# Performance work log

Measured on AMD Instinct MI355X. Metric: run time of the kernel, lower is better.

The kernel has to match this reference:

```python
import jax, jax.numpy as jnp
import numpy as np

B, S, D_IN = 1, 2048, 2048
H, KV, HD = 32, 8, 64          # num_heads, num_kv_groups, head_dim
GS = H // KV                    # group_size
D_OUT = H * HD
EPS = 1e-6


def _rmsnorm(x, w):
    # RMSNormQwen over last dim (head_dim)
    var = jnp.mean(x * x, axis=-1, keepdims=True)
    return x * jax.lax.rsqrt(var + EPS) * w


def _rope(x, cos, sin):
    # rotate-half RoPE; x: [B, heads, S, HD], cos/sin: [S, HD]
    d = x.shape[-1]
    x1, x2 = x[..., : d // 2], x[..., d // 2 :]
    rot = jnp.concatenate([-x2, x1], axis=-1)
    return x * cos + rot * sin


def setup_inputs() -> dict:
    key = jax.random.key(0)
    ks = jax.random.split(key, 8)
    x = jax.random.normal(ks[0], (B, S, D_IN), dtype=jnp.float32)
    Wq = jax.random.normal(ks[1], (D_IN, D_OUT), dtype=jnp.float32) * 0.02
    Wk = jax.random.normal(ks[2], (D_IN, KV * HD), dtype=jnp.float32) * 0.02
    Wv = jax.random.normal(ks[3], (D_IN, KV * HD), dtype=jnp.float32) * 0.02
    Wo = jax.random.normal(ks[4], (D_OUT, D_IN), dtype=jnp.float32) * 0.02
    q_norm_w = jnp.ones((HD,), dtype=jnp.float32)
    k_norm_w = jnp.ones((HD,), dtype=jnp.float32)
    # causal mask: True where masked (j > i)
    mask = jnp.triu(jnp.ones((S, S), dtype=bool), k=1)
    # RoPE tables
    inv_freq = 1.0 / (10000.0 ** (np.arange(0, HD, 2, dtype=np.float32) / HD))
    ang = np.arange(S, dtype=np.float32)[:, None] * inv_freq[None, :]  # [S, HD/2]
    cos = jnp.asarray(np.concatenate([np.cos(ang), np.cos(ang)], axis=-1))
    sin = jnp.asarray(np.concatenate([np.sin(ang), np.sin(ang)], axis=-1))
    return {"x": x, "mask": mask, "cos": cos, "sin": sin,
            "Wq": Wq, "Wk": Wk, "Wv": Wv, "Wo": Wo,
            "q_norm_w": q_norm_w, "k_norm_w": k_norm_w}


def reference(x, mask, cos, sin, Wq, Wk, Wv, Wo, q_norm_w, k_norm_w):
    b, s, _ = x.shape
    q = (x @ Wq).reshape(b, s, H, HD).transpose(0, 2, 1, 3)   # [B,H,S,HD]
    k = (x @ Wk).reshape(b, s, KV, HD).transpose(0, 2, 1, 3)  # [B,KV,S,HD]
    v = (x @ Wv).reshape(b, s, KV, HD).transpose(0, 2, 1, 3)  # [B,KV,S,HD]
    q = _rmsnorm(q, q_norm_w)
    k = _rmsnorm(k, k_norm_w)
    q = _rope(q, cos, sin)
    k = _rope(k, cos, sin)
    # grouped-KV attention without materializing repeated K/V
    qg = q.reshape(b, KV, GS, s, HD)
    scores = jnp.einsum('bkgsd,bktd->bkgst', qg, k)           # [B,KV,GS,S,S]
    scores = jnp.where(mask, -jnp.inf, scores)
    weights = jax.nn.softmax(scores / (HD ** 0.5), axis=-1)
    ctx = jnp.einsum('bkgst,bktd->bkgsd', weights, v)         # [B,KV,GS,S,HD]
    ctx = ctx.reshape(b, H, s, HD).transpose(0, 2, 1, 3).reshape(b, s, D_OUT)
    return ctx @ Wo
```

## Files before the change

kernel.cpp:

```cpp
#include <hip/hip_runtime.h>
#include <hip/hip_bf16.h>
#include <math.h>

#define S_LEN 2048
#define DIN   2048
#define NH    32
#define NKV   8
#define HD    64
#define DOUT  2048
#define QKVN  3072
#define KOFF  2048
#define VOFF  2560

typedef __attribute__((ext_vector_type(8))) short short8v;
typedef __attribute__((ext_vector_type(8))) unsigned short ushort8v;
typedef __attribute__((ext_vector_type(4))) unsigned short ushort4v;
typedef __attribute__((ext_vector_type(4))) float float4v;
typedef __attribute__((ext_vector_type(16))) float float16v;

__device__ __forceinline__ float bf2f(unsigned short u) {
    union { float f; unsigned u; } c; c.u = ((unsigned)u) << 16; return c.f;
}
__device__ __forceinline__ unsigned short f2bf(float f) {
    union { float f; unsigned u; } c; c.f = f;
    unsigned r = c.u + 0x7fffu + ((c.u >> 16) & 1u);
    return (unsigned short)(r >> 16);
}
__device__ __forceinline__ unsigned short f2h(float f) {
    union { _Float16 h; unsigned short u; } c; c.h = (_Float16)f; return c.u;
}
__device__ __forceinline__ float h2f(unsigned short u) {
    union { _Float16 h; unsigned short u; } c; c.u = u; return (float)c.h;
}
__device__ __forceinline__ unsigned cvtpk(float lo, float hi) {
    unsigned r;
    asm("v_cvt_pk_bf16_f32 %0, %1, %2" : "=v"(r) : "v"(lo), "v"(hi));
    return r;
}
__device__ __forceinline__ float fexp2(float x) {
    float r;
    asm("v_exp_f32 %0, %1" : "=v"(r) : "v"(x));
    return r;
}

__global__ __launch_bounds__(256) void prep(const float* __restrict__ Wq,
                                            const float* __restrict__ Wk,
                                            const float* __restrict__ Wv,
                                            const float* __restrict__ Wo,
                                            const float* __restrict__ x,
                                            unsigned short* __restrict__ W1,
                                            unsigned short* __restrict__ WoT,
                                            unsigned short* __restrict__ XB) {
    __shared__ float t[32][33];
    const int a = blockIdx.x;
    const int tx = threadIdx.x & 31, ty = threadIdx.x >> 5;
    if (a < 6144) {
        const int n0 = (a % 96) * 32, k0 = (a / 96) * 32;
        const float* src; int nn0, Nsrc;
        if (n0 < KOFF)      { src = Wq; nn0 = n0;        Nsrc = DOUT; }
        else if (n0 < VOFF) { src = Wk; nn0 = n0 - KOFF; Nsrc = 512; }
        else                { src = Wv; nn0 = n0 - VOFF; Nsrc = 512; }
#pragma unroll
        for (int j = ty; j < 32; j += 8)
            t[j][tx] = src[(size_t)(k0 + j) * Nsrc + nn0 + tx];
        __syncthreads();
#pragma unroll
        for (int j = ty; j < 32; j += 8)
            W1[(size_t)(n0 + j) * DIN + k0 + tx] = f2bf(t[tx][j]);
    } else if (a < 10240) {
        const int b = a - 6144;
        const int n0 = (b % 64) * 32, k0 = (b / 64) * 32;
#pragma unroll
        for (int j = ty; j < 32; j += 8)
            t[j][tx] = Wo[(size_t)(k0 + j) * DIN + n0 + tx];
        __syncthreads();
#pragma unroll
        for (int j = ty; j < 32; j += 8)
            WoT[(size_t)(n0 + j) * DOUT + k0 + tx] = f2bf(t[tx][j]);
    } else {
        const int i = (a - 10240) * 1024 + threadIdx.x * 4;
        float4 v = *(const float4*)(x + i);
        XB[i + 0] = f2bf(v.x); XB[i + 1] = f2bf(v.y);
        XB[i + 2] = f2bf(v.z); XB[i + 3] = f2bf(v.w);
    }
}

template <int FUSE>
__global__ __launch_bounds__(256) void gemm64(const unsigned short* __restrict__ A,
                                              const unsigned short* __restrict__ Bt,
                                              void* __restrict__ Cv, int M, int N, int K,
                                              const float* __restrict__ qnw,
                                              const float* __restrict__ knw,
                                              const float* __restrict__ cosb,
                                              const float* __restrict__ sinb) {
    __shared__ __attribute__((aligned(16))) unsigned short As[2 * 128 * 64];
    __shared__ __attribute__((aligned(16))) unsigned short Bs[2 * 64 * 64];
    const int tid = threadIdx.x, lane = tid & 63, w = tid >> 6;
    const int bm = blockIdx.y * 128, bn = blockIdx.x * 64;
    const int wm = w * 32;

    float4v acc[2][4];
#pragma unroll
    for (int i = 0; i < 2; i++)
#pragma unroll
        for (int j = 0; j < 4; j++) acc[i][j] = (float4v){0.f, 0.f, 0.f, 0.f};

    const int srow = lane >> 3;
    const int schk = (lane & 7) ^ srow;
    const unsigned short* Ag[4];
    const unsigned short* Bg[2];
#pragma unroll
    for (int g = 0; g < 4; g++)
        Ag[g] = A + (size_t)(bm + w * 32 + g * 8 + srow) * K + schk * 8;
#pragma unroll
    for (int g = 0; g < 2; g++)
        Bg[g] = Bt + (size_t)(bn + w * 16 + g * 8 + srow) * K + schk * 8;

    auto STAGE = [&](int t, int b) {
        const size_t ko = (size_t)t * 64;
        unsigned short* Ad = As + b * (128 * 64) + (w * 32) * 64;
        unsigned short* Bd = Bs + b * (64 * 64) + (w * 16) * 64;
#pragma unroll
        for (int g = 0; g < 4; g++)
            __builtin_amdgcn_global_load_lds(
                (const __attribute__((address_space(1))) void*)(Ag[g] + ko),
                (__attribute__((address_space(3))) void*)(Ad + g * 8 * 64), 16, 0, 0);
#pragma unroll
        for (int g = 0; g < 2; g++)
            __builtin_amdgcn_global_load_lds(
                (const __attribute__((address_space(1))) void*)(Bg[g] + ko),
                (__attribute__((address_space(3))) void*)(Bd + g * 8 * 64), 16, 0, 0);
    };

    const int frow = lane & 15, quad = lane >> 4, sw = frow & 7;
    const int NT = K >> 6;

    STAGE(0, 0);

    for (int t = 0; t < NT; t++) {
        const int c = t & 1;
        if (t + 1 < NT) {
            STAGE(t + 1, c ^ 1);
            asm volatile("s_waitcnt vmcnt(6)" ::: "memory");
        } else {
            asm volatile("s_waitcnt vmcnt(0)" ::: "memory");
        }
        __builtin_amdgcn_s_barrier();
        __builtin_amdgcn_sched_barrier(0);

        const unsigned short* Ab = As + c * (128 * 64);
        const unsigned short* Bb = Bs + c * (64 * 64);
        short8v af[2][2], bf[4][2];
#pragma unroll
        for (int fm = 0; fm < 2; fm++)
#pragma unroll
            for (int ks = 0; ks < 2; ks++)
                af[fm][ks] = *(const short8v*)(Ab + (wm + fm * 16 + frow) * 64 +
                                               (((ks * 4 + quad) ^ sw) * 8));
#pragma unroll
        for (int fn = 0; fn < 4; fn++)
#pragma unroll
            for (int ks = 0; ks < 2; ks++)
                bf[fn][ks] = *(const short8v*)(Bb + (fn * 16 + frow) * 64 +
                                               (((ks * 4 + quad) ^ sw) * 8));
        __builtin_amdgcn_s_setprio(1);
#pragma unroll
        for (int ks = 0; ks < 2; ks++)
#pragma unroll
            for (int fm = 0; fm < 2; fm++)
#pragma unroll
                for (int fn = 0; fn < 4; fn++)
                    acc[fm][fn] = __builtin_amdgcn_mfma_f32_16x16x32_bf16(
                        af[fm][ks], bf[fn][ks], acc[fm][fn], 0, 0, 0);
        __builtin_amdgcn_s_setprio(0);

        if (t + 1 < NT) {
            asm volatile("s_waitcnt lgkmcnt(0)" ::: "memory");
            __builtin_amdgcn_sched_barrier(0);
            __builtin_amdgcn_s_barrier();
        }
    }

    const int quad4 = lane >> 4, col16 = lane & 15;
    if constexpr (FUSE == 1) {
        unsigned short* C = (unsigned short*)Cv;
        const int head = bn >> 6;
        if (head < 40) {
            const float* nw = (head < 32) ? qnw : knw;
            float wv[4];
#pragma unroll
            for (int fn = 0; fn < 4; fn++) wv[fn] = nw[fn * 16 + col16];
#pragma unroll
            for (int fm = 0; fm < 2; fm++)
#pragma unroll
                for (int r = 0; r < 4; r++) {
                    float x0 = acc[fm][0][r], x1 = acc[fm][1][r];
                    float x2 = acc[fm][2][r], x3 = acc[fm][3][r];
                    float ss = x0 * x0 + x1 * x1 + x2 * x2 + x3 * x3;
                    ss += __shfl_xor(ss, 1); ss += __shfl_xor(ss, 2);
                    ss += __shfl_xor(ss, 4); ss += __shfl_xor(ss, 8);
                    const float inv = rsqrtf(ss * (1.0f / 64.0f) + 1e-6f);
                    float xn[4] = {x0 * inv * wv[0], x1 * inv * wv[1],
                                   x2 * inv * wv[2], x3 * inv * wv[3]};
                    const int row = bm + wm + fm * 16 + quad4 * 4 + r;
                    const float* cr = cosb + (size_t)row * HD;
                    const float* sr = sinb + (size_t)row * HD;
#pragma unroll
                    for (int fn = 0; fn < 4; fn++) {
                        const float rot = (fn < 2) ? -xn[fn + 2] : xn[fn - 2];
                        const float res = xn[fn] * cr[fn * 16 + col16] +
                                          rot * sr[fn * 16 + col16];
                        C[(size_t)row * N + bn + fn * 16 + col16] = f2bf(res);
                    }
                }
        } else {
#pragma unroll
            for (int fm = 0; fm < 2; fm++)
#pragma unroll
                for (int fn = 0; fn < 4; fn++)
#pragma unroll
                    for (int r = 0; r < 4; r++)
                        C[(size_t)(bm + wm + fm * 16 + quad4 * 4 + r) * N +
                          bn + fn * 16 + col16] = f2bf(acc[fm][fn][r]);
        }
    } else {
        float* C = (float*)Cv;
#pragma unroll
        for (int fm = 0; fm < 2; fm++)
#pragma unroll
            for (int fn = 0; fn < 4; fn++)
#pragma unroll
                for (int r = 0; r < 4; r++)
                    C[(size_t)(bm + wm + fm * 16 + quad4 * 4 + r) * N +
                      bn + fn * 16 + col16] = acc[fm][fn][r];
    }
}

#define KSTR 88

__global__ __launch_bounds__(256, 3) void flash_part(const unsigned short* __restrict__ qb,
                                                     const unsigned short* __restrict__ kb,
                                                     const unsigned short* __restrict__ vb,
                                                     unsigned short* __restrict__ Op,
                                                     float* __restrict__ Lp) {
    __shared__ __attribute__((aligned(16))) unsigned short Ks[2][64 * KSTR];
    __shared__ __attribute__((aligned(16))) unsigned short Vt[2][64 * KSTR];

    const int tid = threadIdx.x, lane = tid & 63, w = tid >> 6;
    const int sl = lane & 31, hi = lane >> 5, hi8 = hi * 8;
    const int bid = blockIdx.x;
    const int g = bid & 7;
    const int p = (bid >> 3) & 31;
    const int c = bid >> 8;
    const int h = g * 4 + w;

    const int s0a = p * 32, s0b = (63 - p) * 32;
    const int nta = (s0a + 95) >> 6;
    const int W0 = c * 11;
    int nA = nta - W0;
    nA = nA < 0 ? 0 : (nA > 11 ? 11 : nA);
    const bool owesA = (c < 2);

    const float C1 = 0.18033688011112042f;
    const float C2 = 12.262908856239697f;

    unsigned short* OhA = Op + (size_t)c * 1024 * DOUT;
    float*          LhA = Lp + (size_t)c * 1024 * NH;
    unsigned short* OhB = Op + (size_t)(2 + c) * 1024 * DOUT;
    float*          LhB = Lp + (size_t)(2 + c) * 1024 * NH;

    int seg = owesA ? 0 : 1;
    int s0 = seg == 0 ? s0a : s0b;

    short8v qf[4];
#pragma unroll
    for (int ksq = 0; ksq < 4; ksq++)
        qf[ksq] = *(const short8v*)(qb + (size_t)(s0 + sl) * QKVN + h * HD +
                                    ksq * 16 + hi8);

    float16v O[2], Lacc;
#pragma unroll
    for (int df = 0; df < 2; df++)
#pragma unroll
        for (int r = 0; r < 16; r++) O[df][r] = 0.f;
#pragma unroll
    for (int r = 0; r < 16; r++) Lacc[r] = 0.f;

    short8v ones;
#pragma unroll
    for (int i = 0; i < 8; i++) ones[i] = (short)0x3F80;

    const int kkey = tid >> 2, kch = tid & 3;
    const unsigned short* kg = kb + (size_t)kkey * QKVN + g * HD + kch * 16;
    const int kp = tid & 31, vdbb = tid >> 5;
    const unsigned short* vg0 = vb + (size_t)(2 * kp) * QKVN + g * HD + vdbb * 8;
    const unsigned short* vg1 = vg0 + QKVN;

    auto epi = [&](int sbase, unsigned short* Os, float* Ls, int roff) {
#pragma unroll
        for (int df = 0; df < 2; df++)
#pragma unroll
            for (int r = 0; r < 16; r++) {
                const int row = sbase + (r & 3) + 8 * (r >> 2) + 4 * hi - roff;
                Os[(size_t)row * DOUT + h * HD + df * 32 + sl] = f2h(O[df][r]);
            }
        if (sl == 0) {
#pragma unroll
            for (int r = 0; r < 16; r++) {
                const int row = sbase + (r & 3) + 8 * (r >> 2) + 4 * hi - roff;
                Ls[(size_t)row * NH + h] = Lacc[r];
            }
        }
    };
    auto zacc = [&]() {
#pragma unroll
        for (int df = 0; df < 2; df++)
#pragma unroll
            for (int r = 0; r < 16; r++) O[df][r] = 0.f;
#pragma unroll
        for (int r = 0; r < 16; r++) Lacc[r] = 0.f;
    };

    auto kt = [&](int jj) {
        const int sj = W0 + jj;
        return (sj < nta) ? sj : (sj - nta);
    };

    ushort8v ka0, ka1, va0, va1;
    auto LOADREGS = [&](int it) {
        const size_t off = (size_t)it * 64 * QKVN;
        ka0 = *(const ushort8v*)(kg + off);
        ka1 = *(const ushort8v*)(kg + off + 8);
        va0 = *(const ushort8v*)(vg0 + off);
        va1 = *(const ushort8v*)(vg1 + off);
    };
    auto COMMIT = [&](int b) {
        unsigned short* kd = Ks[b] + kkey * KSTR + kch * 16;
        *(ushort8v*)kd = ka0;
        *(ushort8v*)(kd + 8) = ka1;
        union { ushort8v v; unsigned d[4]; } ua, ub;
        ua.v = va0; ub.v = va1;
        unsigned short* vd = Vt[b] + (size_t)(vdbb * 8) * KSTR + 2 * kp;
#pragma unroll
        for (int i = 0; i < 8; i++) {
            const unsigned sel = (i & 1) ? 0x07060302u : 0x05040100u;
            const unsigned word = __builtin_amdgcn_perm(ub.d[i >> 1], ua.d[i >> 1], sel);
            *(unsigned*)(vd + (size_t)i * KSTR) = word;
        }
    };

    LOADREGS(kt(0));
    COMMIT(0);
    LOADREGS(kt(1));

#pragma unroll 1
    for (int jj = 0; jj < 11; jj++) {
        const int cur = jj & 1;
        __syncthreads();
        if (jj + 1 < 11) COMMIT(cur ^ 1);
        if (jj + 2 < 11) LOADREGS(kt(jj + 2));
        if (seg == 0 && jj == nA) {
            epi(s0a, OhA, LhA, 0);
            zacc();
            s0 = s0b; seg = 1;
#pragma unroll
            for (int ksq = 0; ksq < 4; ksq++)
                qf[ksq] = *(const short8v*)(qb + (size_t)(s0b + sl) * QKVN +
                                            h * HD + ksq * 16 + hi8);
        }

        const int t0 = kt(jj) * 64;
        const bool edge = (t0 + 63 > s0);

#pragma unroll
        for (int b = 0; b < 2; b++) {
            short8v kf[4];
#pragma unroll
            for (int ksq = 0; ksq < 4; ksq++)
                kf[ksq] = *(const short8v*)(Ks[cur] + (32 * b + sl) * KSTR +
                                            ksq * 16 + hi8);
            float16v sct;
#pragma unroll
            for (int r = 0; r < 16; r++) sct[r] = 0.f;
            __builtin_amdgcn_s_setprio(1);
#pragma unroll
            for (int ksq = 0; ksq < 4; ksq++)
                sct = __builtin_amdgcn_mfma_f32_32x32x16_bf16(kf[ksq], qf[ksq],
                                                              sct, 0, 0, 0);
            __builtin_amdgcn_s_setprio(0);
#pragma unroll
            for (int r = 0; r < 16; r++) {
                float arg = sct[r] * C1 - C2;
                if (edge) {
                    const int kglob = t0 + 32 * b + (r & 3) + 8 * (r >> 2) + 4 * hi;
                    arg = (kglob <= s0 + sl) ? arg : -100.f;
                }
                sct[r] = fexp2(arg);
            }
            unsigned pk[8];
#pragma unroll
            for (int i = 0; i < 8; i++) pk[i] = cvtpk(sct[2 * i], sct[2 * i + 1]);
#pragma unroll
            for (int kk = 0; kk < 2; kk++) {
                unsigned x0 = pk[4 * kk + 0], x1 = pk[4 * kk + 1];
                unsigned y0 = pk[4 * kk + 2], y1 = pk[4 * kk + 3];
                asm("v_permlane32_swap_b32 %0, %1" : "+v"(x0), "+v"(y0));
                asm("v_permlane32_swap_b32 %0, %1" : "+v"(x1), "+v"(y1));
                union { unsigned u[4]; short8v v; } pa;
                pa.u[0] = x0; pa.u[1] = x1; pa.u[2] = y0; pa.u[3] = y1;
                const int ks = 2 * b + kk;
                __builtin_amdgcn_s_setprio(1);
#pragma unroll
                for (int df = 0; df < 2; df++) {
                    const short8v vf = *(const short8v*)(Vt[cur] +
                                                         (size_t)(df * 32 + sl) * KSTR +
                                                         ks * 16 + hi8);
                    O[df] = __builtin_amdgcn_mfma_f32_32x32x16_bf16(pa.v, vf,
                                                                    O[df], 0, 0, 0);
                }
                Lacc = __builtin_amdgcn_mfma_f32_32x32x16_bf16(pa.v, ones,
                                                               Lacc, 0, 0, 0);
                __builtin_amdgcn_s_setprio(0);
            }
        }
    }

    if (seg == 0) {
        epi(s0a, OhA, LhA, 0);
        zacc();
    }
    epi(s0b, OhB, LhB, 1024);
}

__global__ __launch_bounds__(256) void combine(const unsigned short* __restrict__ Op,
                                               const float* __restrict__ Lp,
                                               unsigned short* __restrict__ CTX) {
    const int i4 = (blockIdx.x * 256 + threadIdx.x) * 4;
    const int row = i4 >> 11, hh = (i4 & 2047) >> 6;
    float acc[4];
    float l;
    if (row < 1024) {
        ushort4v a0 = *(const ushort4v*)(Op + i4);
        ushort4v a1 = *(const ushort4v*)(Op + (size_t)1024 * DOUT + i4);
#pragma unroll
        for (int j = 0; j < 4; j++) acc[j] = h2f(a0[j]) + h2f(a1[j]);
        l = Lp[(size_t)row * NH + hh] + Lp[(size_t)(1024 + row) * NH + hh];
    } else {
        const size_t j4 = (size_t)(row - 1024) * DOUT + (i4 & 2047);
        ushort4v b0 = *(const ushort4v*)(Op + (size_t)2 * 1024 * DOUT + j4);
        ushort4v b1 = *(const ushort4v*)(Op + (size_t)3 * 1024 * DOUT + j4);
        ushort4v b2 = *(const ushort4v*)(Op + (size_t)4 * 1024 * DOUT + j4);
#pragma unroll
        for (int j = 0; j < 4; j++) acc[j] = h2f(b0[j]) + h2f(b1[j]) + h2f(b2[j]);
        const size_t lr = (size_t)(row - 1024) * NH + hh;
        l = Lp[(size_t)2 * 1024 * NH + lr] + Lp[(size_t)3 * 1024 * NH + lr] +
            Lp[(size_t)4 * 1024 * NH + lr];
    }
    const float inv = 1.0f / l;
    ushort4v r;
#pragma unroll
    for (int j = 0; j < 4; j++) r[j] = f2bf(acc[j] * inv);
    *(ushort4v*)(CTX + i4) = r;
}

extern "C" void kernel_launch(void* const* d_in, const int* in_sizes, int n_in,
                              void* d_out, int out_size, void* d_ws, size_t ws_size,
                              hipStream_t stream) {
    const float* x    = (const float*)d_in[0];
    const float* cosb = (const float*)d_in[2];
    const float* sinb = (const float*)d_in[3];
    const float* Wq   = (const float*)d_in[4];
    const float* Wk   = (const float*)d_in[5];
    const float* Wv   = (const float*)d_in[6];
    const float* Wo   = (const float*)d_in[7];
    const float* qw   = (const float*)d_in[8];
    const float* kw   = (const float*)d_in[9];
    float* out = (float*)d_out;

    unsigned short* W1  = (unsigned short*)d_ws;
    unsigned short* XB  = W1 + (size_t)QKVN * DIN;
    unsigned short* WoT = XB + (size_t)S_LEN * DIN;
    unsigned short* QKV = WoT + (size_t)DIN * DOUT;
    unsigned short* Op  = (unsigned short*)d_ws;
    float*          Lp  = (float*)d_out;
    unsigned short* CTX = QKV;

    dim3 blk256(256);

    prep<<<dim3(14336), blk256, 0, stream>>>(Wq, Wk, Wv, Wo, x, W1, WoT, XB);

    gemm64<1><<<dim3(QKVN / 64, S_LEN / 128), blk256, 0, stream>>>(
        XB, W1, QKV, S_LEN, QKVN, DIN, qw, kw, cosb, sinb);

    flash_part<<<dim3(NKV * 32 * 3), blk256, 0, stream>>>(
        QKV, QKV + KOFF, QKV + VOFF, Op, Lp);

    combine<<<dim3(S_LEN * DOUT / 1024), blk256, 0, stream>>>(Op, Lp, CTX);

    gemm64<0><<<dim3(DIN / 64, S_LEN / 128), blk256, 0, stream>>>(
        CTX, WoT, out, S_LEN, DIN, DOUT, nullptr, nullptr, nullptr, nullptr);
}
```

Measured before the change: 235.4 us.

## Split flash attention KV work into four chunks and raise occupancy

Changes the split-KV partitioning from three chunks of 11 tiles to four chunks (9,8,8,8), launching 1024 blocks instead of 768 so more CUs stay busy and each block does less serial work. Shrinks the LDS row stride from 88 to 72 and raises launch bounds to four blocks per CU to increase occupancy. The extra partial output is staged in the output buffer, and the combine kernel now sums four partials for the second half. The trade-offs are more partial-output traffic in combine, possible LDS bank conflicts with the new stride, and register pressure from the higher occupancy target.

Measured after the change: 251.5 us. 1.07x slower.

```diff
diff --git a/kernel.cpp b/kernel.cpp
--- a/kernel.cpp
+++ b/kernel.cpp
@@ -236,12 +236,13 @@
     }
 }
 
-#define KSTR 88
-
-__global__ __launch_bounds__(256, 3) void flash_part(const unsigned short* __restrict__ qb,
+#define KSTR 72
+
+__global__ __launch_bounds__(256, 4) void flash_part(const unsigned short* __restrict__ qb,
                                                      const unsigned short* __restrict__ kb,
                                                      const unsigned short* __restrict__ vb,
-                                                     unsigned short* __restrict__ Op,
+                                                     unsigned short* __restrict__ OpW,
+                                                     unsigned short* __restrict__ OpD,
                                                      float* __restrict__ Lp) {
     __shared__ __attribute__((aligned(16))) unsigned short Ks[2][64 * KSTR];
     __shared__ __attribute__((aligned(16))) unsigned short Vt[2][64 * KSTR];
@@ -254,22 +255,23 @@
     const int c = bid >> 8;
     const int h = g * 4 + w;
 
+    const int co   = c ? (9 + (c - 1) * 8) : 0;
+    const int clen = c ? 8 : 9;
+
     const int s0a = p * 32, s0b = (63 - p) * 32;
     const int nta = (s0a + 95) >> 6;
-    const int W0 = c * 11;
-    int nA = nta - W0;
-    nA = nA < 0 ? 0 : (nA > 11 ? 11 : nA);
-    const bool owesA = (c < 2);
+    int nA = nta - co;
+    nA = nA < 0 ? 0 : (nA > clen ? clen : nA);
 
     const float C1 = 0.18033688011112042f;
     const float C2 = 12.262908856239697f;
 
-    unsigned short* OhA = Op + (size_t)c * 1024 * DOUT;
+    unsigned short* OhA = OpW + (size_t)c * 1024 * DOUT;
     float*          LhA = Lp + (size_t)c * 1024 * NH;
-    unsigned short* OhB = Op + (size_t)(2 + c) * 1024 * DOUT;
+    unsigned short* OhB = (c < 3) ? (OpW + (size_t)(2 + c) * 1024 * DOUT) : OpD;
     float*          LhB = Lp + (size_t)(2 + c) * 1024 * NH;
 
-    int seg = owesA ? 0 : 1;
+    int seg = (c < 2) ? 0 : 1;
     int s0 = seg == 0 ? s0a : s0b;
 
     short8v qf[4];
@@ -322,7 +324,7 @@
     };
 
     auto kt = [&](int jj) {
-        const int sj = W0 + jj;
+        const int sj = co + jj;
         return (sj < nta) ? sj : (sj - nta);
     };
 
@@ -354,11 +356,11 @@
     LOADREGS(kt(1));
 
 #pragma unroll 1
-    for (int jj = 0; jj < 11; jj++) {
+    for (int jj = 0; jj < clen; jj++) {
         const int cur = jj & 1;
         __syncthreads();
-        if (jj + 1 < 11) COMMIT(cur ^ 1);
-        if (jj + 2 < 11) LOADREGS(kt(jj + 2));
+        if (jj + 1 < clen) COMMIT(cur ^ 1);
+        if (jj + 2 < clen) LOADREGS(kt(jj + 2));
         if (seg == 0 && jj == nA) {
             epi(s0a, OhA, LhA, 0);
             zacc();
@@ -432,7 +434,8 @@
     epi(s0b, OhB, LhB, 1024);
 }
 
-__global__ __launch_bounds__(256) void combine(const unsigned short* __restrict__ Op,
+__global__ __launch_bounds__(256) void combine(const unsigned short* __restrict__ OpW,
+                                               const unsigned short* __restrict__ OpD,
                                                const float* __restrict__ Lp,
                                                unsigned short* __restrict__ CTX) {
     const int i4 = (blockIdx.x * 256 + threadIdx.x) * 4;
@@ -440,21 +443,23 @@
     float acc[4];
     float l;
     if (row < 1024) {
-        ushort4v a0 = *(const ushort4v*)(Op + i4);
-        ushort4v a1 = *(const ushort4v*)(Op + (size_t)1024 * DOUT + i4);
+        ushort4v a0 = *(const ushort4v*)(OpW + i4);
+        ushort4v a1 = *(const ushort4v*)(OpW + (size_t)1024 * DOUT + i4);
 #pragma unroll
         for (int j = 0; j < 4; j++) acc[j] = h2f(a0[j]) + h2f(a1[j]);
         l = Lp[(size_t)row * NH + hh] + Lp[(size_t)(1024 + row) * NH + hh];
     } else {
         const size_t j4 = (size_t)(row - 1024) * DOUT + (i4 & 2047);
-        ushort4v b0 = *(const ushort4v*)(Op + (size_t)2 * 1024 * DOUT + j4);
-        ushort4v b1 = *(const ushort4v*)(Op + (size_t)3 * 1024 * DOUT + j4);
-        ushort4v b2 = *(const ushort4v*)(Op + (size_t)4 * 1024 * DOUT + j4);
-#pragma unroll
-        for (int j = 0; j < 4; j++) acc[j] = h2f(b0[j]) + h2f(b1[j]) + h2f(b2[j]);
+        ushort4v b0 = *(const ushort4v*)(OpW + (size_t)2 * 1024 * DOUT + j4);
+        ushort4v b1 = *(const ushort4v*)(OpW + (size_t)3 * 1024 * DOUT + j4);
+        ushort4v b2 = *(const ushort4v*)(OpW + (size_t)4 * 1024 * DOUT + j4);
+        ushort4v b3 = *(const ushort4v*)(OpD + j4);
+#pragma unroll
+        for (int j = 0; j < 4; j++)
+            acc[j] = (h2f(b0[j]) + h2f(b1[j])) + (h2f(b2[j]) + h2f(b3[j]));
         const size_t lr = (size_t)(row - 1024) * NH + hh;
-        l = Lp[(size_t)2 * 1024 * NH + lr] + Lp[(size_t)3 * 1024 * NH + lr] +
-            Lp[(size_t)4 * 1024 * NH + lr];
+        l = (Lp[(size_t)2 * 1024 * NH + lr] + Lp[(size_t)3 * 1024 * NH + lr]) +
+            (Lp[(size_t)4 * 1024 * NH + lr] + Lp[(size_t)5 * 1024 * NH + lr]);
     }
     const float inv = 1.0f / l;
     ushort4v r;
@@ -481,8 +486,9 @@
     unsigned short* XB  = W1 + (size_t)QKVN * DIN;
     unsigned short* WoT = XB + (size_t)S_LEN * DIN;
     unsigned short* QKV = WoT + (size_t)DIN * DOUT;
-    unsigned short* Op  = (unsigned short*)d_ws;
-    float*          Lp  = (float*)d_out;
+    unsigned short* OpW = (unsigned short*)d_ws;
+    unsigned short* OpD = (unsigned short*)d_out;
+    float*          Lp  = (float*)(OpD + (size_t)1024 * DOUT);
     unsigned short* CTX = QKV;
 
     dim3 blk256(256);
@@ -492,10 +498,10 @@
     gemm64<1><<<dim3(QKVN / 64, S_LEN / 128), blk256, 0, stream>>>(
         XB, W1, QKV, S_LEN, QKVN, DIN, qw, kw, cosb, sinb);
 
-    flash_part<<<dim3(NKV * 32 * 3), blk256, 0, stream>>>(
-        QKV, QKV + KOFF, QKV + VOFF, Op, Lp);
-
-    combine<<<dim3(S_LEN * DOUT / 1024), blk256, 0, stream>>>(Op, Lp, CTX);
+    flash_part<<<dim3(NKV * 32 * 4), blk256, 0, stream>>>(
+        QKV, QKV + KOFF, QKV + VOFF, OpW, OpD, Lp);
+
+    combine<<<dim3(S_LEN * DOUT / 1024), blk256, 0, stream>>>(OpW, OpD, Lp, CTX);
 
     gemm64<0><<<dim3(DIN / 64, S_LEN / 128), blk256, 0, stream>>>(
         CTX, WoT, out, S_LEN, DIN, DOUT, nullptr, nullptr, nullptr, nullptr);
```
